# Kernel optimization log

Hardware: AMD Instinct MI355X
Metric: run time of the kernel (lower is better)

The kernel has to match this reference:

```python
import jax, jax.numpy as jnp
import numpy as np


def setup_inputs() -> dict:
    key = jax.random.key(0)
    ks = jax.random.split(key, 8)
    B, C, H, W = 8, 256, 64, 64
    s = 1.0 / np.sqrt(C)
    return {
        "x": jax.random.normal(ks[0], (B, C, H, W), dtype=jnp.float32),
        "wq": jax.random.normal(ks[1], (C, C), dtype=jnp.float32) * s,
        "bq": jax.random.normal(ks[2], (C,), dtype=jnp.float32) * 0.01,
        "wk": jax.random.normal(ks[3], (C, C), dtype=jnp.float32) * s,
        "bk": jax.random.normal(ks[4], (C,), dtype=jnp.float32) * 0.01,
        "wv": jax.random.normal(ks[5], (C, C), dtype=jnp.float32) * s,
        "bv": jax.random.normal(ks[6], (C,), dtype=jnp.float32) * 0.01,
        "gamma": jax.random.normal(ks[7], (1,), dtype=jnp.float32) * 0.1,
    }


def reference(x, wq, bq, wk, bk, wv, bv, gamma):
    B, C, H, W = x.shape
    N = H * W
    xf = x.reshape(B, C, N)  # flatten spatial -> tokens
    # 1x1 convs == per-pixel linear maps over channels
    q = jnp.einsum('oc,bcn->bon', wq, xf) + bq[None, :, None]  # [B,C,N]
    k = jnp.einsum('oc,bcn->bon', wk, xf) + bk[None, :, None]  # [B,C,N]
    v = jnp.einsum('oc,bcn->bon', wv, xf) + bv[None, :, None]  # [B,C,N]
    # energy[b,n,m] = <q[:, n], k[:, m]>  (query tokens x key tokens)
    energy = jnp.einsum('bcn,bcm->bnm', q, k)  # [B,N,N]
    attention = jax.nn.softmax(energy, axis=-1)
    # out = V @ attention^T : out[b,c,n] = sum_m v[b,c,m] * attention[b,n,m]
    out = jnp.einsum('bcm,bnm->bcn', v, attention).reshape(B, C, H, W)
    return gamma[0] * out + x
```

## Files before the change

### kernel.cpp

```cpp
#include <hip/hip_runtime.h>
#include <hip/hip_bf16.h>
#include <cstdint>


typedef short short8 __attribute__((ext_vector_type(8)));
typedef short short4v __attribute__((ext_vector_type(4)));
typedef float f32x4 __attribute__((ext_vector_type(4)));
typedef unsigned int uint4v __attribute__((ext_vector_type(4)));

#define MFMA16(a, b, c) __builtin_amdgcn_mfma_f32_16x16x32_bf16((a), (b), (c), 0, 0, 0)
#define LOG2E 1.4426950408889634f

__device__ __forceinline__ unsigned short f2bf(float f) {
    union { float f; unsigned int u; } v;
    v.f = f;
    unsigned int u = v.u;
    return (unsigned short)((u + 0x7fffu + ((u >> 16) & 1u)) >> 16);
}

__device__ __forceinline__ void load_lds16(const unsigned short* g, unsigned short* l) {
    __builtin_amdgcn_global_load_lds(
        (const __attribute__((address_space(1))) unsigned int*)g,
        (__attribute__((address_space(3))) unsigned int*)l, 16, 0, 0);
}

__device__ __forceinline__ float rowmax16_dpp(float x) {
    int v;
    v = __builtin_amdgcn_update_dpp(0, __float_as_int(x), 0x121, 0xf, 0xf, false);
    x = fmaxf(x, __int_as_float(v));
    v = __builtin_amdgcn_update_dpp(0, __float_as_int(x), 0x122, 0xf, 0xf, false);
    x = fmaxf(x, __int_as_float(v));
    v = __builtin_amdgcn_update_dpp(0, __float_as_int(x), 0x124, 0xf, 0xf, false);
    x = fmaxf(x, __int_as_float(v));
    v = __builtin_amdgcn_update_dpp(0, __float_as_int(x), 0x128, 0xf, 0xf, false);
    x = fmaxf(x, __int_as_float(v));
    return x;
}

__device__ __forceinline__ float wavemax_bcast(float x) {
    int v;
    v = __builtin_amdgcn_update_dpp(__float_as_int(x), __float_as_int(x), 0x142, 0xf, 0xf, false);
    x = fmaxf(x, __int_as_float(v));
    v = __builtin_amdgcn_update_dpp(__float_as_int(x), __float_as_int(x), 0x143, 0xf, 0xf, false);
    x = fmaxf(x, __int_as_float(v));
    return __int_as_float(__builtin_amdgcn_readlane(__float_as_int(x), 63));
}

__global__ __launch_bounds__(256) void wcvt_kernel(
    const float* __restrict__ wq, const float* __restrict__ wk,
    const float* __restrict__ wv, unsigned short* __restrict__ Wb)
{
    int idx = (blockIdx.x * 256 + threadIdx.x) * 4;
    const float* src = (idx < 65536) ? wq : ((idx < 131072) ? wk : wv);
    float4 f = *(const float4*)(src + (idx & 65535));
    short4v s = { (short)f2bf(f.x), (short)f2bf(f.y), (short)f2bf(f.z), (short)f2bf(f.w) };
    *(short4v*)(Wb + idx) = s;
}

__global__ __launch_bounds__(256, 2) void qkv_kernel(
    const float* __restrict__ x, const unsigned short* __restrict__ Wb,
    const float* __restrict__ bq, const float* __restrict__ bk,
    const float* __restrict__ bv,
    unsigned short* __restrict__ Qc, unsigned short* __restrict__ Kr,
    unsigned short* __restrict__ Vc)
{
    const int C = 256, N = 4096;
    __shared__ __align__(16) unsigned short Xt[32][264];

    const int tid  = threadIdx.x;
    const int bid  = blockIdx.x;
    const int b    = bid >> 7;
    const int n0   = (bid & 127) * 32;
    const int wave = tid >> 6;
    const int lane = tid & 63;
    const int quad = lane >> 4;
    const int l16  = lane & 15;
    const int ch0  = wave * 64;

    {
        const int token = tid & 31;
        const int cg    = tid >> 5;
        const float* xb = x + ((size_t)b * C) * N + n0 + token;
#pragma unroll
        for (int p = 0; p < 8; p++) {
            int c0 = p * 32 + cg * 4;
            float f0 = xb[(size_t)(c0 + 0) * N];
            float f1 = xb[(size_t)(c0 + 1) * N];
            float f2 = xb[(size_t)(c0 + 2) * N];
            float f3 = xb[(size_t)(c0 + 3) * N];
            short4v s = { (short)f2bf(f0), (short)f2bf(f1), (short)f2bf(f2), (short)f2bf(f3) };
            *(short4v*)(&Xt[token][c0]) = s;
        }
    }
    __syncthreads();

    f32x4 acc[4][2];

#pragma unroll
    for (int ct = 0; ct < 4; ct++)
#pragma unroll
        for (int tt = 0; tt < 2; tt++) acc[ct][tt] = (f32x4){0.f, 0.f, 0.f, 0.f};
#pragma unroll
    for (int kc = 0; kc < 8; kc++) {
        const int ko = kc * 32 + quad * 8;
        short8 ax0 = *(const short8*)(&Xt[l16][ko]);
        short8 ax1 = *(const short8*)(&Xt[16 + l16][ko]);
#pragma unroll
        for (int ct = 0; ct < 4; ct++) {
            short8 wf = *(const short8*)(Wb + (ch0 + ct * 16 + l16) * 256 + ko);
            acc[ct][0] = MFMA16(ax0, wf, acc[ct][0]);
            acc[ct][1] = MFMA16(ax1, wf, acc[ct][1]);
        }
    }
#pragma unroll
    for (int ct = 0; ct < 4; ct++) {
        const int ch = ch0 + ct * 16 + l16;
        const float biq = bq[ch];
#pragma unroll
        for (int tt = 0; tt < 2; tt++) {
            const int tok0 = n0 + tt * 16 + quad * 4;
            short4v qs = { (short)f2bf((acc[ct][tt][0] + biq) * LOG2E),
                           (short)f2bf((acc[ct][tt][1] + biq) * LOG2E),
                           (short)f2bf((acc[ct][tt][2] + biq) * LOG2E),
                           (short)f2bf((acc[ct][tt][3] + biq) * LOG2E) };
            *(short4v*)(Qc + ((size_t)b * C + ch) * N + tok0) = qs;
        }
    }

#pragma unroll
    for (int ct = 0; ct < 4; ct++)
#pragma unroll
        for (int tt = 0; tt < 2; tt++) acc[ct][tt] = (f32x4){0.f, 0.f, 0.f, 0.f};
#pragma unroll
    for (int kc = 0; kc < 8; kc++) {
        const int ko = kc * 32 + quad * 8;
        short8 ax0 = *(const short8*)(&Xt[l16][ko]);
        short8 ax1 = *(const short8*)(&Xt[16 + l16][ko]);
#pragma unroll
        for (int ct = 0; ct < 4; ct++) {
            short8 wf = *(const short8*)(Wb + (2 << 16) + (ch0 + ct * 16 + l16) * 256 + ko);
            acc[ct][0] = MFMA16(ax0, wf, acc[ct][0]);
            acc[ct][1] = MFMA16(ax1, wf, acc[ct][1]);
        }
    }
#pragma unroll
    for (int ct = 0; ct < 4; ct++) {
        const int ch = ch0 + ct * 16 + l16;
        const float biv = bv[ch];
        uint4v vv;
#pragma unroll
        for (int r = 0; r < 4; r++) {
            unsigned int lo = f2bf(acc[ct][0][r] + biv);
            unsigned int hi = f2bf(acc[ct][1][r] + biv);
            vv[r] = lo | (hi << 16);
        }
        *(uint4v*)(Vc + ((size_t)b * C + ch) * N + n0 + quad * 8) = vv;
    }

#pragma unroll
    for (int ct = 0; ct < 4; ct++)
#pragma unroll
        for (int tt = 0; tt < 2; tt++) acc[ct][tt] = (f32x4){0.f, 0.f, 0.f, 0.f};
#pragma unroll
    for (int kc = 0; kc < 8; kc++) {
        const int ko = kc * 32 + quad * 8;
        short8 ax0 = *(const short8*)(&Xt[l16][ko]);
        short8 ax1 = *(const short8*)(&Xt[16 + l16][ko]);
#pragma unroll
        for (int ct = 0; ct < 4; ct++) {
            short8 wf = *(const short8*)(Wb + (1 << 16) + (ch0 + ct * 16 + l16) * 256 + ko);
            acc[ct][0] = MFMA16(ax0, wf, acc[ct][0]);
            acc[ct][1] = MFMA16(ax1, wf, acc[ct][1]);
        }
    }
    __syncthreads();
#pragma unroll
    for (int ct = 0; ct < 4; ct++) {
        const int ch = ch0 + ct * 16 + l16;
        const float bik = bk[ch];
#pragma unroll
        for (int tt = 0; tt < 2; tt++) {
#pragma unroll
            for (int r = 0; r < 4; r++)
                Xt[tt * 16 + quad * 4 + r][ch] = f2bf(acc[ct][tt][r] + bik);
        }
    }
    __syncthreads();
#pragma unroll
    for (int p = 0; p < 2; p++) {
        int chunk = p * 256 + tid;
        int tok = chunk >> 4;
        int cc  = (chunk & 15) * 16;
        *(short8*)(Kr + ((size_t)b * N + n0 + tok) * C + cc) = *(const short8*)(&Xt[tok][cc]);
    }
}

__global__ __launch_bounds__(512, 2) void attn_kernel(
    const unsigned short* __restrict__ Qc,
    const unsigned short* __restrict__ Kr,
    const unsigned short* __restrict__ Vc,
    const float* __restrict__ x,
    const float* __restrict__ gamma,
    float* __restrict__ out)
{
    const int C = 256, N = 4096;
    __shared__ __align__(16) unsigned short KV[2][32768];
    __shared__ __align__(16) unsigned int P32[8][32][16];
    __shared__ float MlL[4][32];
    __shared__ float MwL[4];

    const int tid  = threadIdx.x;
    const int wave = tid >> 6;
    const int ks   = wave >> 2;
    const int w4   = wave & 3;
    const int lane = tid & 63;
    const int quad = lane >> 4;
    const int l16  = lane & 15;
    const int bid  = blockIdx.x;
    const int b    = bid & 7;
    const int q0   = (bid >> 3) * 128 + w4 * 32;

    const unsigned short* kb  = Kr + (size_t)b * N * C;
    const unsigned short* vcb = Vc + (size_t)b * C * N;

    short8 aqL[8], aqH[8];
    {
        const unsigned short* qb = Qc + (size_t)b * C * N + q0 + l16;
#pragma unroll
        for (int f = 0; f < 8; f++) {
#pragma unroll
            for (int j = 0; j < 8; j++) {
                size_t co = (size_t)(f * 32 + quad * 8 + j) * N;
                aqL[f][j] = (short)qb[co];
                aqH[f][j] = (short)qb[co + 16];
            }
        }
    }

    f32x4 oL[16], oH[16];
#pragma unroll
    for (int t = 0; t < 16; t++) {
        oL[t] = (f32x4){0.f, 0.f, 0.f, 0.f};
        oH[t] = (f32x4){0.f, 0.f, 0.f, 0.f};
    }
    float m_w = -__builtin_inff();
    float l_p[2][4];
#pragma unroll
    for (int h = 0; h < 2; h++)
#pragma unroll
        for (int r = 0; r < 4; r++) l_p[h][r] = 0.f;

    auto stage = [&](int buf, int m0) {
        unsigned short* dst = &KV[buf][0];
#pragma unroll
        for (int p = 0; p < 4; p++) {
            int chunk = p * 512 + tid;
            int half = chunk >> 10;
            int idx  = chunk & 1023;
            int key = idx >> 5;
            int j = (idx & 31) ^ (key & 31);
            load_lds16(kb + (size_t)(half * 2048 + m0 + key) * C + j * 8,
                       dst + half * 16384 + idx * 8);
        }
#pragma unroll
        for (int p = 0; p < 4; p++) {
            int chunk = p * 512 + tid;
            int half = chunk >> 10;
            int idx  = chunk & 1023;
            int c = idx >> 2;
            int j = (idx & 3) ^ (c & 3);
            load_lds16(vcb + (size_t)c * N + half * 2048 + m0 + j * 8,
                       dst + half * 16384 + 8192 + idx * 8);
        }
    };

    stage(0, 0);
    __syncthreads();

    unsigned int* PtW = &P32[wave][0][0];

    for (int it = 0; it < 64; ++it) {
        const int cur = it & 1;
        if (it < 63) stage(cur ^ 1, (it + 1) * 32);

        const unsigned short* Kb = &KV[cur][ks * 16384];
        const unsigned short* Vb = Kb + 8192;

        f32x4 sL0 = {0.f,0.f,0.f,0.f}, sL1 = {0.f,0.f,0.f,0.f};
        f32x4 sH0 = {0.f,0.f,0.f,0.f}, sH1 = {0.f,0.f,0.f,0.f};
#pragma unroll
        for (int f = 0; f < 8; f++) {
            const int j = f * 4 + quad;
            int k0 = l16, k1 = 16 + l16;
            short8 kf0 = *(const short8*)(Kb + (k0 * 32 + (j ^ (k0 & 31))) * 8);
            short8 kf1 = *(const short8*)(Kb + (k1 * 32 + (j ^ (k1 & 31))) * 8);
            sL0 = MFMA16(aqL[f], kf0, sL0);
            sL1 = MFMA16(aqL[f], kf1, sL1);
            sH0 = MFMA16(aqH[f], kf0, sH0);
            sH1 = MFMA16(aqH[f], kf1, sH1);
        }

        float mx = fmaxf(fmaxf(fmaxf(sL0[0], sL0[1]), fmaxf(sL0[2], sL0[3])),
                         fmaxf(fmaxf(sL1[0], sL1[1]), fmaxf(sL1[2], sL1[3])));
        mx = fmaxf(mx, fmaxf(fmaxf(fmaxf(sH0[0], sH0[1]), fmaxf(sH0[2], sH0[3])),
                             fmaxf(fmaxf(sH1[0], sH1[1]), fmaxf(sH1[2], sH1[3]))));
        mx = rowmax16_dpp(mx);
        mx = wavemax_bcast(mx);
        const float mn = fmaxf(m_w, mx);
        const float al = exp2f(m_w - mn);
        const bool up = mn > m_w;
        m_w = mn;

#pragma unroll
        for (int r = 0; r < 4; r++) {
            {
                float e0 = exp2f(sL0[r] - mn);
                float e1 = exp2f(sL1[r] - mn);
                l_p[0][r] = l_p[0][r] * al + (e0 + e1);
                union { __hip_bfloat162 v; unsigned int u; } cv;
                cv.v = __float22bfloat162_rn(float2{e0, e1});
                PtW[(quad * 4 + r) * 16 + l16] = cv.u;
            }
            {
                float e0 = exp2f(sH0[r] - mn);
                float e1 = exp2f(sH1[r] - mn);
                l_p[1][r] = l_p[1][r] * al + (e0 + e1);
                union { __hip_bfloat162 v; unsigned int u; } cv;
                cv.v = __float22bfloat162_rn(float2{e0, e1});
                PtW[(16 + quad * 4 + r) * 16 + l16] = cv.u;
            }
        }
        if (up) {
#pragma unroll
            for (int t = 0; t < 16; t++) { oL[t] *= al; oH[t] *= al; }
        }

        short8 apL = *(const short8*)(PtW + l16 * 16 + quad * 4);
        short8 apH = *(const short8*)(PtW + (16 + l16) * 16 + quad * 4);

#pragma unroll
        for (int t = 0; t < 16; t++) {
            int c = t * 16 + l16;
            short8 vf = *(const short8*)(Vb + (c * 4 + (quad ^ (c & 3))) * 8);
            oL[t] = MFMA16(apL, vf, oL[t]);
            oH[t] = MFMA16(apH, vf, oH[t]);
        }
        __syncthreads();
    }

#pragma unroll
    for (int h = 0; h < 2; h++)
#pragma unroll
        for (int r = 0; r < 4; r++) {
            float rs = l_p[h][r];
            rs += __shfl_xor(rs, 1);
            rs += __shfl_xor(rs, 2);
            rs += __shfl_xor(rs, 4);
            rs += __shfl_xor(rs, 8);
            l_p[h][r] = rs;
        }

    float* CombF = (float*)(&KV[0][0]);
    __syncthreads();
    if (ks == 1) {
#pragma unroll
        for (int t = 0; t < 16; t++) {
#pragma unroll
            for (int r = 0; r < 4; r++) {
                CombF[(size_t)(w4 * 32 + quad * 4 + r) * 256 + t * 16 + l16] = oL[t][r];
                CombF[(size_t)(w4 * 32 + 16 + quad * 4 + r) * 256 + t * 16 + l16] = oH[t][r];
            }
        }
        if (l16 == 0) {
#pragma unroll
            for (int h = 0; h < 2; h++)
#pragma unroll
                for (int r = 0; r < 4; r++)
                    MlL[w4][h * 16 + quad * 4 + r] = l_p[h][r];
            if (lane == 0) MwL[w4] = m_w;
        }
    }
    __syncthreads();
    if (ks == 0) {
        const float g = gamma[0];
        const float m2w = MwL[w4];
        const float mt = fmaxf(m_w, m2w);
        const float f1 = exp2f(m_w - mt);
        const float f2 = exp2f(m2w - mt);
        float linv[2][4];
#pragma unroll
        for (int h = 0; h < 2; h++)
#pragma unroll
            for (int r = 0; r < 4; r++) {
                float l2 = MlL[w4][h * 16 + quad * 4 + r];
                linv[h][r] = g / (l_p[h][r] * f1 + l2 * f2);
            }
#pragma unroll
        for (int t = 0; t < 16; t++) {
            const int c = t * 16 + l16;
#pragma unroll
            for (int h = 0; h < 2; h++) {
                const int nb = q0 + h * 16 + quad * 4;
                f32x4 o1 = h ? oH[t] : oL[t];
                f32x4 ov;
#pragma unroll
                for (int r = 0; r < 4; r++) {
                    float o2 = CombF[(size_t)(w4 * 32 + h * 16 + quad * 4 + r) * 256 + c];
                    ov[r] = (o1[r] * f1 + o2 * f2) * linv[h][r];
                }
                size_t idx = ((size_t)(b * C + c)) * N + nb;
                f32x4 xv = *(const f32x4*)(x + idx);
                *(f32x4*)(out + idx) = ov + xv;
            }
        }
    }
}

extern "C" void kernel_launch(void* const* d_in, const int* in_sizes, int n_in,
                              void* d_out, int out_size, void* d_ws, size_t ws_size,
                              hipStream_t stream) {
    const int B = 8, C = 256, N = 4096;
    const float* x     = (const float*)d_in[0];
    const float* wq    = (const float*)d_in[1];
    const float* bq    = (const float*)d_in[2];
    const float* wk    = (const float*)d_in[3];
    const float* bk    = (const float*)d_in[4];
    const float* wv    = (const float*)d_in[5];
    const float* bv    = (const float*)d_in[6];
    const float* gamma = (const float*)d_in[7];
    float* out = (float*)d_out;

    unsigned short* Qc = (unsigned short*)d_ws;
    unsigned short* Kr = Qc + (size_t)B * C * N;
    unsigned short* Vc = Kr + (size_t)B * N * C;
    unsigned short* Wb = Vc + (size_t)B * C * N;

    wcvt_kernel<<<dim3(192), 256, 0, stream>>>(wq, wk, wv, Wb);
    qkv_kernel<<<dim3(1024), 256, 0, stream>>>(x, Wb, bq, bk, bv, Qc, Kr, Vc);
    attn_kernel<<<dim3(256), 512, 0, stream>>>(Qc, Kr, Vc, x, gamma, out);
}
```

Measured before the change: 380.1 us.

## Interleave Q token layout, precompute stage addresses, lazy softmax rescale, MFMA priority

Q is now written with the token pairs n and n+16 packed into one 32-bit word, so the attention kernel loads both query halves with a single 32-bit gather instead of two 16-bit loads. The K/V staging addresses are computed once and advanced by pointer increments rather than recomputed on every iteration. The online softmax now rescales the accumulators only when the running max rises by more than 8 in log2 units, which skips most rescales at some risk to float range. It also changes the P LDS layout to cut bank conflicts and raises wave priority around the MFMA loops with s_setprio.

```diff
diff --git a/kernel.cpp b/kernel.cpp
--- a/kernel.cpp
+++ b/kernel.cpp
@@ -116,15 +116,14 @@
     for (int ct = 0; ct < 4; ct++) {
         const int ch = ch0 + ct * 16 + l16;
         const float biq = bq[ch];
-#pragma unroll
-        for (int tt = 0; tt < 2; tt++) {
-            const int tok0 = n0 + tt * 16 + quad * 4;
-            short4v qs = { (short)f2bf((acc[ct][tt][0] + biq) * LOG2E),
-                           (short)f2bf((acc[ct][tt][1] + biq) * LOG2E),
-                           (short)f2bf((acc[ct][tt][2] + biq) * LOG2E),
-                           (short)f2bf((acc[ct][tt][3] + biq) * LOG2E) };
-            *(short4v*)(Qc + ((size_t)b * C + ch) * N + tok0) = qs;
-        }
+        uint4v qv;
+#pragma unroll
+        for (int r = 0; r < 4; r++) {
+            unsigned int lo = f2bf((acc[ct][0][r] + biq) * LOG2E);
+            unsigned int hi = f2bf((acc[ct][1][r] + biq) * LOG2E);
+            qv[r] = lo | (hi << 16);
+        }
+        *(uint4v*)(Qc + ((size_t)b * C + ch) * N + n0 + quad * 8) = qv;
     }
 
 #pragma unroll
@@ -225,14 +224,15 @@
 
     short8 aqL[8], aqH[8];
     {
-        const unsigned short* qb = Qc + (size_t)b * C * N + q0 + l16;
+        const unsigned int* qb32 = (const unsigned int*)(Qc + (size_t)b * C * N);
 #pragma unroll
         for (int f = 0; f < 8; f++) {
 #pragma unroll
             for (int j = 0; j < 8; j++) {
-                size_t co = (size_t)(f * 32 + quad * 8 + j) * N;
-                aqL[f][j] = (short)qb[co];
-                aqH[f][j] = (short)qb[co + 16];
+                size_t i32 = ((size_t)(f * 32 + quad * 8 + j) * N + q0) / 2 + l16;
+                unsigned int u = qb32[i32];
+                aqL[f][j] = (short)(u & 0xffff);
+                aqH[f][j] = (short)(u >> 16);
             }
         }
     }
@@ -250,44 +250,60 @@
 #pragma unroll
         for (int r = 0; r < 4; r++) l_p[h][r] = 0.f;
 
-    auto stage = [&](int buf, int m0) {
+    const unsigned short* srcK[4];
+    const unsigned short* srcV[4];
+    int dstK[4], dstV[4];
+#pragma unroll
+    for (int p = 0; p < 4; p++) {
+        int chunk = p * 512 + tid;
+        int half = chunk >> 10;
+        int idx  = chunk & 1023;
+        int key = idx >> 5;
+        int j = (idx & 31) ^ (key & 31);
+        srcK[p] = kb + (size_t)(half * 2048 + key) * C + j * 8;
+        dstK[p] = half * 16384 + idx * 8;
+    }
+#pragma unroll
+    for (int p = 0; p < 4; p++) {
+        int chunk = p * 512 + tid;
+        int half = chunk >> 10;
+        int idx  = chunk & 1023;
+        int c = idx >> 2;
+        int j = (idx & 3) ^ (c & 3);
+        srcV[p] = vcb + (size_t)c * N + half * 2048 + j * 8;
+        dstV[p] = half * 16384 + 8192 + idx * 8;
+    }
+
+    auto stage = [&](int buf) {
         unsigned short* dst = &KV[buf][0];
 #pragma unroll
-        for (int p = 0; p < 4; p++) {
-            int chunk = p * 512 + tid;
-            int half = chunk >> 10;
-            int idx  = chunk & 1023;
-            int key = idx >> 5;
-            int j = (idx & 31) ^ (key & 31);
-            load_lds16(kb + (size_t)(half * 2048 + m0 + key) * C + j * 8,
-                       dst + half * 16384 + idx * 8);
-        }
-#pragma unroll
-        for (int p = 0; p < 4; p++) {
-            int chunk = p * 512 + tid;
-            int half = chunk >> 10;
-            int idx  = chunk & 1023;
-            int c = idx >> 2;
-            int j = (idx & 3) ^ (c & 3);
-            load_lds16(vcb + (size_t)c * N + half * 2048 + m0 + j * 8,
-                       dst + half * 16384 + 8192 + idx * 8);
-        }
+        for (int p = 0; p < 4; p++) load_lds16(srcK[p], dst + dstK[p]);
+#pragma unroll
+        for (int p = 0; p < 4; p++) load_lds16(srcV[p], dst + dstV[p]);
     };
-
-    stage(0, 0);
+    auto advance = [&]() {
+#pragma unroll
+        for (int p = 0; p < 4; p++) { srcK[p] += 32 * C; srcV[p] += 32; }
+    };
+
+    stage(0);
+    advance();
     __syncthreads();
 
     unsigned int* PtW = &P32[wave][0][0];
+    const int prL = (((l16 >> 2) + 8 * (l16 & 3)) << 4) + quad * 4;
+    const int prH = prL + 64;
 
     for (int it = 0; it < 64; ++it) {
         const int cur = it & 1;
-        if (it < 63) stage(cur ^ 1, (it + 1) * 32);
+        if (it < 63) { stage(cur ^ 1); advance(); }
 
         const unsigned short* Kb = &KV[cur][ks * 16384];
         const unsigned short* Vb = Kb + 8192;
 
         f32x4 sL0 = {0.f,0.f,0.f,0.f}, sL1 = {0.f,0.f,0.f,0.f};
         f32x4 sH0 = {0.f,0.f,0.f,0.f}, sH1 = {0.f,0.f,0.f,0.f};
+        __builtin_amdgcn_s_setprio(1);
 #pragma unroll
         for (int f = 0; f < 8; f++) {
             const int j = f * 4 + quad;
@@ -299,6 +315,7 @@
             sH0 = MFMA16(aqH[f], kf0, sH0);
             sH1 = MFMA16(aqH[f], kf1, sH1);
         }
+        __builtin_amdgcn_s_setprio(0);
 
         float mx = fmaxf(fmaxf(fmaxf(sL0[0], sL0[1]), fmaxf(sL0[2], sL0[3])),
                          fmaxf(fmaxf(sL1[0], sL1[1]), fmaxf(sL1[2], sL1[3])));
@@ -306,38 +323,43 @@
                              fmaxf(fmaxf(sH1[0], sH1[1]), fmaxf(sH1[2], sH1[3]))));
         mx = rowmax16_dpp(mx);
         mx = wavemax_bcast(mx);
-        const float mn = fmaxf(m_w, mx);
-        const float al = exp2f(m_w - mn);
-        const bool up = mn > m_w;
-        m_w = mn;
+
+        if (mx > m_w + 8.0f) {
+            const float al = exp2f(m_w - mx);
+            m_w = mx;
+#pragma unroll
+            for (int h = 0; h < 2; h++)
+#pragma unroll
+                for (int r = 0; r < 4; r++) l_p[h][r] *= al;
+#pragma unroll
+            for (int t = 0; t < 16; t++) { oL[t] *= al; oH[t] *= al; }
+        }
+        const float mn = m_w;
 
 #pragma unroll
         for (int r = 0; r < 4; r++) {
             {
                 float e0 = exp2f(sL0[r] - mn);
                 float e1 = exp2f(sL1[r] - mn);
-                l_p[0][r] = l_p[0][r] * al + (e0 + e1);
+                l_p[0][r] += e0 + e1;
                 union { __hip_bfloat162 v; unsigned int u; } cv;
                 cv.v = __float22bfloat162_rn(float2{e0, e1});
-                PtW[(quad * 4 + r) * 16 + l16] = cv.u;
+                PtW[((quad + 8 * r) << 4) + l16] = cv.u;
             }
             {
                 float e0 = exp2f(sH0[r] - mn);
                 float e1 = exp2f(sH1[r] - mn);
-                l_p[1][r] = l_p[1][r] * al + (e0 + e1);
+                l_p[1][r] += e0 + e1;
                 union { __hip_bfloat162 v; unsigned int u; } cv;
                 cv.v = __float22bfloat162_rn(float2{e0, e1});
-                PtW[(16 + quad * 4 + r) * 16 + l16] = cv.u;
-            }
-        }
-        if (up) {
-#pragma unroll
-            for (int t = 0; t < 16; t++) { oL[t] *= al; oH[t] *= al; }
-        }
-
-        short8 apL = *(const short8*)(PtW + l16 * 16 + quad * 4);
-        short8 apH = *(const short8*)(PtW + (16 + l16) * 16 + quad * 4);
-
+                PtW[((quad + 4 + 8 * r) << 4) + l16] = cv.u;
+            }
+        }
+
+        short8 apL = *(const short8*)(PtW + prL);
+        short8 apH = *(const short8*)(PtW + prH);
+
+        __builtin_amdgcn_s_setprio(1);
 #pragma unroll
         for (int t = 0; t < 16; t++) {
             int c = t * 16 + l16;
@@ -345,6 +367,7 @@
             oL[t] = MFMA16(apL, vf, oL[t]);
             oH[t] = MFMA16(apH, vf, oH[t]);
         }
+        __builtin_amdgcn_s_setprio(0);
         __syncthreads();
     }
 
```

Result: slower. 401.1 us (+5.5%).

## Compute transposed scores so softmax probabilities feed PV MFMA from registers

Applied to the files above, without the earlier changes.

Swaps the MFMA operand order in the QK^T product so the score tile comes out transposed. Each lane then holds exactly the probability fragment the PV MFMA needs, which removes the per-wave LDS round-trip through P32. Q is now stored with token pairs interleaved so it loads as 32-bit words, and row sums are reduced with cross-quad shuffles. A lazy rescale applies the new running max only when it exceeds the old one by more than 8 (log2 units), cutting exp and accumulator multiplies at some risk of larger bf16 probabilities.

```diff
diff --git a/kernel.cpp b/kernel.cpp
--- a/kernel.cpp
+++ b/kernel.cpp
@@ -116,15 +116,14 @@
     for (int ct = 0; ct < 4; ct++) {
         const int ch = ch0 + ct * 16 + l16;
         const float biq = bq[ch];
-#pragma unroll
-        for (int tt = 0; tt < 2; tt++) {
-            const int tok0 = n0 + tt * 16 + quad * 4;
-            short4v qs = { (short)f2bf((acc[ct][tt][0] + biq) * LOG2E),
-                           (short)f2bf((acc[ct][tt][1] + biq) * LOG2E),
-                           (short)f2bf((acc[ct][tt][2] + biq) * LOG2E),
-                           (short)f2bf((acc[ct][tt][3] + biq) * LOG2E) };
-            *(short4v*)(Qc + ((size_t)b * C + ch) * N + tok0) = qs;
-        }
+        uint4v qv;
+#pragma unroll
+        for (int r = 0; r < 4; r++) {
+            unsigned int lo = f2bf((acc[ct][0][r] + biq) * LOG2E);
+            unsigned int hi = f2bf((acc[ct][1][r] + biq) * LOG2E);
+            qv[r] = lo | (hi << 16);
+        }
+        *(uint4v*)(Qc + ((size_t)b * C + ch) * N + n0 + quad * 8) = qv;
     }
 
 #pragma unroll
@@ -205,8 +204,7 @@
 {
     const int C = 256, N = 4096;
     __shared__ __align__(16) unsigned short KV[2][32768];
-    __shared__ __align__(16) unsigned int P32[8][32][16];
-    __shared__ float MlL[4][32];
+    __shared__ float Lw[8][32];
     __shared__ float MwL[4];
 
     const int tid  = threadIdx.x;
@@ -225,14 +223,15 @@
 
     short8 aqL[8], aqH[8];
     {
-        const unsigned short* qb = Qc + (size_t)b * C * N + q0 + l16;
+        const unsigned int* qb32 = (const unsigned int*)(Qc + (size_t)b * C * N);
 #pragma unroll
         for (int f = 0; f < 8; f++) {
 #pragma unroll
             for (int j = 0; j < 8; j++) {
-                size_t co = (size_t)(f * 32 + quad * 8 + j) * N;
-                aqL[f][j] = (short)qb[co];
-                aqH[f][j] = (short)qb[co + 16];
+                size_t i32 = ((size_t)(f * 32 + quad * 8 + j) * N + q0) / 2 + l16;
+                unsigned int u = qb32[i32];
+                aqL[f][j] = (short)(u & 0xffff);
+                aqH[f][j] = (short)(u >> 16);
             }
         }
     }
@@ -244,11 +243,7 @@
         oH[t] = (f32x4){0.f, 0.f, 0.f, 0.f};
     }
     float m_w = -__builtin_inff();
-    float l_p[2][4];
-#pragma unroll
-    for (int h = 0; h < 2; h++)
-#pragma unroll
-        for (int r = 0; r < 4; r++) l_p[h][r] = 0.f;
+    float l_pL = 0.f, l_pH = 0.f;
 
     auto stage = [&](int buf, int m0) {
         unsigned short* dst = &KV[buf][0];
@@ -277,8 +272,6 @@
     stage(0, 0);
     __syncthreads();
 
-    unsigned int* PtW = &P32[wave][0][0];
-
     for (int it = 0; it < 64; ++it) {
         const int cur = it & 1;
         if (it < 63) stage(cur ^ 1, (it + 1) * 32);
@@ -286,57 +279,57 @@
         const unsigned short* Kb = &KV[cur][ks * 16384];
         const unsigned short* Vb = Kb + 8192;
 
-        f32x4 sL0 = {0.f,0.f,0.f,0.f}, sL1 = {0.f,0.f,0.f,0.f};
-        f32x4 sH0 = {0.f,0.f,0.f,0.f}, sH1 = {0.f,0.f,0.f,0.f};
+        f32x4 tL0 = {0.f,0.f,0.f,0.f}, tL1 = {0.f,0.f,0.f,0.f};
+        f32x4 tH0 = {0.f,0.f,0.f,0.f}, tH1 = {0.f,0.f,0.f,0.f};
 #pragma unroll
         for (int f = 0; f < 8; f++) {
             const int j = f * 4 + quad;
             int k0 = l16, k1 = 16 + l16;
             short8 kf0 = *(const short8*)(Kb + (k0 * 32 + (j ^ (k0 & 31))) * 8);
             short8 kf1 = *(const short8*)(Kb + (k1 * 32 + (j ^ (k1 & 31))) * 8);
-            sL0 = MFMA16(aqL[f], kf0, sL0);
-            sL1 = MFMA16(aqL[f], kf1, sL1);
-            sH0 = MFMA16(aqH[f], kf0, sH0);
-            sH1 = MFMA16(aqH[f], kf1, sH1);
-        }
-
-        float mx = fmaxf(fmaxf(fmaxf(sL0[0], sL0[1]), fmaxf(sL0[2], sL0[3])),
-                         fmaxf(fmaxf(sL1[0], sL1[1]), fmaxf(sL1[2], sL1[3])));
-        mx = fmaxf(mx, fmaxf(fmaxf(fmaxf(sH0[0], sH0[1]), fmaxf(sH0[2], sH0[3])),
-                             fmaxf(fmaxf(sH1[0], sH1[1]), fmaxf(sH1[2], sH1[3]))));
+            tL0 = MFMA16(kf0, aqL[f], tL0);
+            tL1 = MFMA16(kf1, aqL[f], tL1);
+            tH0 = MFMA16(kf0, aqH[f], tH0);
+            tH1 = MFMA16(kf1, aqH[f], tH1);
+        }
+
+        float mx = fmaxf(fmaxf(fmaxf(tL0[0], tL0[1]), fmaxf(tL0[2], tL0[3])),
+                         fmaxf(fmaxf(tL1[0], tL1[1]), fmaxf(tL1[2], tL1[3])));
+        mx = fmaxf(mx, fmaxf(fmaxf(fmaxf(tH0[0], tH0[1]), fmaxf(tH0[2], tH0[3])),
+                             fmaxf(fmaxf(tH1[0], tH1[1]), fmaxf(tH1[2], tH1[3]))));
         mx = rowmax16_dpp(mx);
         mx = wavemax_bcast(mx);
-        const float mn = fmaxf(m_w, mx);
-        const float al = exp2f(m_w - mn);
-        const bool up = mn > m_w;
-        m_w = mn;
-
-#pragma unroll
-        for (int r = 0; r < 4; r++) {
-            {
-                float e0 = exp2f(sL0[r] - mn);
-                float e1 = exp2f(sL1[r] - mn);
-                l_p[0][r] = l_p[0][r] * al + (e0 + e1);
-                union { __hip_bfloat162 v; unsigned int u; } cv;
-                cv.v = __float22bfloat162_rn(float2{e0, e1});
-                PtW[(quad * 4 + r) * 16 + l16] = cv.u;
-            }
-            {
-                float e0 = exp2f(sH0[r] - mn);
-                float e1 = exp2f(sH1[r] - mn);
-                l_p[1][r] = l_p[1][r] * al + (e0 + e1);
-                union { __hip_bfloat162 v; unsigned int u; } cv;
-                cv.v = __float22bfloat162_rn(float2{e0, e1});
-                PtW[(16 + quad * 4 + r) * 16 + l16] = cv.u;
-            }
-        }
-        if (up) {
+
+        if (mx > m_w + 8.0f) {
+            const float al = exp2f(m_w - mx);
+            m_w = mx;
+            l_pL *= al; l_pH *= al;
 #pragma unroll
             for (int t = 0; t < 16; t++) { oL[t] *= al; oH[t] *= al; }
         }
-
-        short8 apL = *(const short8*)(PtW + l16 * 16 + quad * 4);
-        short8 apH = *(const short8*)(PtW + (16 + l16) * 16 + quad * 4);
+        const float mn = m_w;
+
+        uint4v apLu, apHu;
+#pragma unroll
+        for (int w = 0; w < 4; w++) {
+            float e0 = exp2f(tL0[w] - mn);
+            float e1 = exp2f(tL1[w] - mn);
+            l_pL += e0 + e1;
+            union { __hip_bfloat162 v; unsigned int u; } cv;
+            cv.v = __float22bfloat162_rn(float2{e0, e1});
+            apLu[w] = cv.u;
+            float g0 = exp2f(tH0[w] - mn);
+            float g1 = exp2f(tH1[w] - mn);
+            l_pH += g0 + g1;
+            union { __hip_bfloat162 v; unsigned int u; } cw;
+            cw.v = __float22bfloat162_rn(float2{g0, g1});
+            apHu[w] = cw.u;
+        }
+        short8 apL, apH;
+        {
+            union { uint4v u; short8 s; } c1; c1.u = apLu; apL = c1.s;
+            union { uint4v u; short8 s; } c2; c2.u = apHu; apH = c2.s;
+        }
 
 #pragma unroll
         for (int t = 0; t < 16; t++) {
@@ -348,17 +341,14 @@
         __syncthreads();
     }
 
-#pragma unroll
-    for (int h = 0; h < 2; h++)
-#pragma unroll
-        for (int r = 0; r < 4; r++) {
-            float rs = l_p[h][r];
-            rs += __shfl_xor(rs, 1);
-            rs += __shfl_xor(rs, 2);
-            rs += __shfl_xor(rs, 4);
-            rs += __shfl_xor(rs, 8);
-            l_p[h][r] = rs;
-        }
+    l_pL += __shfl_xor(l_pL, 16);
+    l_pL += __shfl_xor(l_pL, 32);
+    l_pH += __shfl_xor(l_pH, 16);
+    l_pH += __shfl_xor(l_pH, 32);
+    if (quad == 0) {
+        Lw[wave][l16] = l_pL;
+        Lw[wave][16 + l16] = l_pH;
+    }
 
     float* CombF = (float*)(&KV[0][0]);
     __syncthreads();
@@ -371,14 +361,7 @@
                 CombF[(size_t)(w4 * 32 + 16 + quad * 4 + r) * 256 + t * 16 + l16] = oH[t][r];
             }
         }
-        if (l16 == 0) {
-#pragma unroll
-            for (int h = 0; h < 2; h++)
-#pragma unroll
-                for (int r = 0; r < 4; r++)
-                    MlL[w4][h * 16 + quad * 4 + r] = l_p[h][r];
-            if (lane == 0) MwL[w4] = m_w;
-        }
+        if (lane == 0) MwL[w4] = m_w;
     }
     __syncthreads();
     if (ks == 0) {
@@ -392,8 +375,8 @@
         for (int h = 0; h < 2; h++)
 #pragma unroll
             for (int r = 0; r < 4; r++) {
-                float l2 = MlL[w4][h * 16 + quad * 4 + r];
-                linv[h][r] = g / (l_p[h][r] * f1 + l2 * f2);
+                const int q = h * 16 + quad * 4 + r;
+                linv[h][r] = g / (Lw[w4][q] * f1 + Lw[4 + w4][q] * f2);
             }
 #pragma unroll
         for (int t = 0; t < 16; t++) {
```

Measured after the change: 367.6 us. 3.3% less time.
